# Optimization experiments

Measured on AMD Instinct MI355X. Metric: run time of the kernel, lower is better.

## Reference

```python
import jax, jax.numpy as jnp
import numpy as np

NEG_SLOPE = 0.2
K_NN = 3


def gat_conv(x, edge_index, W, a_src, a_dst, b):
    """PyG GATConv (heads=1, add_self_loops=True).
    x: [N, F_in]; edge_index: [2, E] (row0=src, row1=dst)."""
    n = x.shape[0]
    loops = jnp.arange(n)
    src = jnp.concatenate([edge_index[0], loops])
    dst = jnp.concatenate([edge_index[1], loops])
    h = x @ W                                   # [N, H]
    a_s = h @ a_src                             # [N] per-node src score
    a_d = h @ a_dst                             # [N] per-node dst score
    e = jax.nn.leaky_relu(a_s[src] + a_d[dst], NEG_SLOPE)  # [E+N]
    # segment softmax over edges sharing the same destination
    e_max = jax.ops.segment_max(e, dst, num_segments=n)
    ex = jnp.exp(e - e_max[dst])
    denom = jax.ops.segment_sum(ex, dst, num_segments=n)
    alpha = ex / denom[dst]
    out = jax.ops.segment_sum(alpha[:, None] * h[src], dst, num_segments=n)
    return out + b


def knn_pool(x_resting, x_collider):
    """For each collider node find K_NN nearest resting nodes (L2), then
    scatter_mean collider features onto resting nodes."""
    nr = x_resting.shape[0]
    nc = x_collider.shape[0]
    # squared distances [Nc, Nr]
    d2 = (jnp.sum(x_collider ** 2, -1, keepdims=True)
          - 2.0 * (x_collider @ x_resting.T)
          + jnp.sum(x_resting ** 2, -1)[None, :])
    _, idx = jax.lax.top_k(-d2, K_NN)           # [Nc, K] resting indices
    row = idx.reshape(-1)                        # resting index per knn edge
    col = jnp.repeat(jnp.arange(nc), K_NN)       # collider index per knn edge
    feats = x_collider[col]                      # [Nc*K, H]
    sums = jax.ops.segment_sum(feats, row, num_segments=nr)
    cnt = jax.ops.segment_sum(jnp.ones((nc * K_NN,), feats.dtype), row,
                              num_segments=nr)
    return sums / jnp.maximum(cnt, 1.0)[:, None]


def setup_inputs() -> dict:
    key = jax.random.key(0)
    ks = jax.random.split(key, 20)
    Nr, Nc, Er, Ec = 10000, 5000, 160000, 80000
    Fr, Fc, H, O = 3, 6, 128, 3
    s = 0.1
    inp = {
        "x_resting": jax.random.normal(ks[0], (Nr, Fr), jnp.float32),
        "edge_index_resting": jax.random.randint(ks[1], (2, Er), 0, Nr),
        "x_collider": jax.random.normal(ks[2], (Nc, Fc), jnp.float32),
        "edge_index_collider": jax.random.randint(ks[3], (2, Ec), 0, Nc),
        # conv1_resting
        "W1r": jax.random.normal(ks[4], (Fr, H), jnp.float32) * s,
        "as1r": jax.random.normal(ks[5], (H,), jnp.float32) * s,
        "ad1r": jax.random.normal(ks[6], (H,), jnp.float32) * s,
        "b1r": jnp.zeros((H,), jnp.float32),
        # conv2_resting
        "W2r": jax.random.normal(ks[7], (H, H), jnp.float32) * s,
        "as2r": jax.random.normal(ks[8], (H,), jnp.float32) * s,
        "ad2r": jax.random.normal(ks[9], (H,), jnp.float32) * s,
        "b2r": jnp.zeros((H,), jnp.float32),
        # conv1_collider
        "W1c": jax.random.normal(ks[10], (Fc, H), jnp.float32) * s,
        "as1c": jax.random.normal(ks[11], (H,), jnp.float32) * s,
        "ad1c": jax.random.normal(ks[12], (H,), jnp.float32) * s,
        "b1c": jnp.zeros((H,), jnp.float32),
        # conv2_collider
        "W2c": jax.random.normal(ks[13], (H, H), jnp.float32) * s,
        "as2c": jax.random.normal(ks[14], (H,), jnp.float32) * s,
        "ad2c": jax.random.normal(ks[15], (H,), jnp.float32) * s,
        "b2c": jnp.zeros((H,), jnp.float32),
        # decoder
        "Wd": jax.random.normal(ks[16], (2 * H, O), jnp.float32) * s,
        "bd": jnp.zeros((O,), jnp.float32),
    }
    return inp


def reference(x_resting, edge_index_resting, x_collider, edge_index_collider,
              W1r, as1r, ad1r, b1r, W2r, as2r, ad2r, b2r,
              W1c, as1c, ad1c, b1c, W2c, as2c, ad2c, b2c, Wd, bd):
    # resting branch (dropout is identity in eval mode)
    hr = jax.nn.relu(gat_conv(x_resting, edge_index_resting, W1r, as1r, ad1r, b1r))
    hr = jax.nn.relu(gat_conv(hr, edge_index_resting, W2r, as2r, ad2r, b2r))
    # collider branch
    hc = jax.nn.relu(gat_conv(x_collider, edge_index_collider, W1c, as1c, ad1c, b1c))
    hc = jax.nn.relu(gat_conv(hc, edge_index_collider, W2c, as2c, ad2c, b2c))
    pooled = knn_pool(hr, hc)                    # [Nr, H]
    x_combined = jnp.concatenate([hr, pooled], axis=-1)
    x_out = x_combined @ Wd + bd                 # new node positions [Nr, 3]
    return x_out
```

## Files before the change

kernel.cpp:

```cpp
#include <hip/hip_runtime.h>
#include <hip/hip_bf16.h>
#include <cstdint>
#include <cstddef>

#define DI __device__ __forceinline__

DI float lrelu(float x) { return x > 0.f ? x : 0.2f * x; }
DI int clampi(int v, int lo, int hi) { return v < lo ? lo : (v > hi ? hi : v); }
DI float clampf(float v) { return fminf(fmaxf(v, -1e15f), 1e15f); }

DI float ldm(const void* p, int i, int mode) {
    if (mode) return ((const float*)p)[i];
    return __bfloat162float(((const __hip_bfloat16*)p)[i]);
}

DI void ins3(float v, int ix, float bv[3], int bi[3]) {
    bool b2 = (v < bv[2]) || (v == bv[2] && ix < bi[2]);
    if (!b2) return;
    bool b0 = (v < bv[0]) || (v == bv[0] && ix < bi[0]);
    bool b1 = (v < bv[1]) || (v == bv[1] && ix < bi[1]);
    if (b0) {
        bv[2] = bv[1]; bi[2] = bi[1];
        bv[1] = bv[0]; bi[1] = bi[0];
        bv[0] = v;     bi[0] = ix;
    } else if (b1) {
        bv[2] = bv[1]; bi[2] = bi[1];
        bv[1] = v;     bi[1] = ix;
    } else {
        bv[2] = v;     bi[2] = ix;
    }
}

__global__ void k_detect(const unsigned short* __restrict__ u, int n, int* __restrict__ flag) {
    int i = blockIdx.x * 256 + threadIdx.x;
    if (i < n) {
        if (((u[i] >> 7) & 0xFF) == 0xFF) atomicOr(flag, 1);
    }
}

__global__ void k_hist(const int* __restrict__ dst, int E, int* __restrict__ deg, int N) {
    int e = blockIdx.x * 256 + threadIdx.x;
    if (e < E) {
        unsigned d = (unsigned)dst[e];
        if (d < (unsigned)N) atomicAdd(&deg[d], 1);
    }
}

__global__ __launch_bounds__(1024) void k_scan(const int* __restrict__ deg, int* __restrict__ off, int N) {
    __shared__ int s[1024];
    __shared__ int carry_s;
    int tid = threadIdx.x;
    if (tid == 0) carry_s = 0;
    __syncthreads();
    for (int base = 0; base < N; base += 1024) {
        int i = base + tid;
        int v = (i < N) ? deg[i] : 0;
        s[tid] = v;
        __syncthreads();
        for (int d = 1; d < 1024; d <<= 1) {
            int t = (tid >= d) ? s[tid - d] : 0;
            __syncthreads();
            s[tid] += t;
            __syncthreads();
        }
        if (i < N) off[i] = carry_s + s[tid] - v;
        int tot = s[1023];
        __syncthreads();
        if (tid == 0) carry_s += tot;
        __syncthreads();
    }
    if (tid == 0) off[N] = carry_s;
}

__global__ void k_scatter(const int* __restrict__ src, const int* __restrict__ dst, int E,
                          const int* __restrict__ off, int* __restrict__ cur, int* __restrict__ sorted,
                          int N) {
    int e = blockIdx.x * 256 + threadIdx.x;
    if (e < E) {
        unsigned d = (unsigned)dst[e];
        if (d < (unsigned)N) {
            int p = off[d] + atomicAdd(&cur[d], 1);
            sorted[p] = clampi(src[e], 0, N - 1);
        }
    }
}

template <int FIN>
__global__ __launch_bounds__(128) void k_lin(const void* __restrict__ x,
                                             const void* __restrict__ W,
                                             const void* __restrict__ av_src,
                                             const void* __restrict__ av_dst,
                                             const int* __restrict__ mode_p,
                                             float* __restrict__ h, float* __restrict__ as_,
                                             float* __restrict__ ad_, int N) {
    int mode = *mode_p;
    int n = blockIdx.x;
    int f = threadIdx.x;
    __shared__ float xs[FIN];
    if (f < FIN) xs[f] = ldm(x, n * FIN + f, mode);
    __syncthreads();
    float acc = 0.f;
#pragma unroll
    for (int k = 0; k < FIN; k++) acc += xs[k] * ldm(W, k * 128 + f, mode);
    acc = clampf(acc);
    h[(size_t)n * 128 + f] = acc;
    __shared__ float r1[128], r2[128];
    r1[f] = acc * ldm(av_src, f, mode);
    r2[f] = acc * ldm(av_dst, f, mode);
    __syncthreads();
    for (int s2 = 64; s2 > 0; s2 >>= 1) {
        if (f < s2) { r1[f] += r1[f + s2]; r2[f] += r2[f + s2]; }
        __syncthreads();
    }
    if (f == 0) { as_[n] = clampf(r1[0]); ad_[n] = clampf(r2[0]); }
}

__global__ __launch_bounds__(128) void k_lin_f32(const float* __restrict__ x,
                                                 const void* __restrict__ W,
                                                 const void* __restrict__ av_src,
                                                 const void* __restrict__ av_dst,
                                                 const int* __restrict__ mode_p,
                                                 float* __restrict__ h, float* __restrict__ as_,
                                                 float* __restrict__ ad_, int N) {
    int mode = *mode_p;
    int n = blockIdx.x;
    int f = threadIdx.x;
    __shared__ float xs[128];
    xs[f] = x[(size_t)n * 128 + f];
    __syncthreads();
    float acc = 0.f;
#pragma unroll
    for (int k = 0; k < 128; k++) acc += xs[k] * ldm(W, k * 128 + f, mode);
    acc = clampf(acc);
    h[(size_t)n * 128 + f] = acc;
    __shared__ float r1[128], r2[128];
    r1[f] = acc * ldm(av_src, f, mode);
    r2[f] = acc * ldm(av_dst, f, mode);
    __syncthreads();
    for (int s2 = 64; s2 > 0; s2 >>= 1) {
        if (f < s2) { r1[f] += r1[f + s2]; r2[f] += r2[f + s2]; }
        __syncthreads();
    }
    if (f == 0) { as_[n] = clampf(r1[0]); ad_[n] = clampf(r2[0]); }
}

__global__ __launch_bounds__(256) void k_agg(const float* __restrict__ h, const float* __restrict__ as_,
                                             const float* __restrict__ ad_, const int* __restrict__ off,
                                             const int* __restrict__ sorted,
                                             const void* __restrict__ bias,
                                             const int* __restrict__ mode_p,
                                             float* __restrict__ out, int N) {
    int mode = *mode_p;
    int w = (blockIdx.x * blockDim.x + threadIdx.x) >> 6;
    int lane = threadIdx.x & 63;
    if (w >= N) return;
    int s0 = off[w], s1 = off[w + 1];
    float adv = ad_[w];
    float eself = lrelu(as_[w] + adv);
    float m = eself;
    for (int j = s0 + lane; j < s1; j += 64) {
        int s = clampi(sorted[j], 0, N - 1);
        m = fmaxf(m, lrelu(as_[s] + adv));
    }
#pragma unroll
    for (int d = 32; d > 0; d >>= 1) m = fmaxf(m, __shfl_xor(m, d, 64));
    const float2* h2 = (const float2*)h;
    float wself = __expf(eself - m);
    float denom = wself;
    float2 hv = h2[(size_t)w * 64 + lane];
    float a0 = wself * hv.x, a1 = wself * hv.y;
    for (int j = s0; j < s1; j++) {
        int s = clampi(sorted[j], 0, N - 1);
        float wj = __expf(lrelu(as_[s] + adv) - m);
        denom += wj;
        float2 hs = h2[(size_t)s * 64 + lane];
        a0 += wj * hs.x;
        a1 += wj * hs.y;
    }
    float inv = 1.f / fmaxf(denom, 1e-30f);
    float o0 = a0 * inv + ldm(bias, lane * 2, mode);
    float o1 = a1 * inv + ldm(bias, lane * 2 + 1, mode);
    out[(size_t)w * 128 + lane * 2] = fminf(fmaxf(o0, 0.f), 1e15f);
    out[(size_t)w * 128 + lane * 2 + 1] = fminf(fmaxf(o1, 0.f), 1e15f);
}

__global__ __launch_bounds__(256) void k_norm(const float* __restrict__ hr, float* __restrict__ rn, int N) {
    int w = (blockIdx.x * blockDim.x + threadIdx.x) >> 6;
    int lane = threadIdx.x & 63;
    if (w >= N) return;
    const float2* h2 = (const float2*)hr;
    float2 v = h2[(size_t)w * 64 + lane];
    float s = v.x * v.x + v.y * v.y;
#pragma unroll
    for (int d = 32; d > 0; d >>= 1) s += __shfl_xor(s, d, 64);
    if (lane == 0) rn[w] = s;
}

#define KNN_TC 64
#define KNN_TR 128
#define KNN_NCH 16
#define KNN_STRIDE 36

__global__ __launch_bounds__(256)
void k_knn_part(const float* __restrict__ hr,
                const float* __restrict__ hc,
                const float* __restrict__ rn,
                float* __restrict__ cand_v, int* __restrict__ cand_i,
                int NR, int NC, int chunk) {
    __shared__ float lds[(KNN_TC + KNN_TR) * KNN_STRIDE];
    float* hcs = lds;
    float* hrs = lds + KNN_TC * KNN_STRIDE;
    int tid = threadIdx.x;
    int tx = tid & 7;
    int ty = tid >> 3;
    int c0 = blockIdx.x * KNN_TC;
    int rbase = blockIdx.y * chunk;
    int rend = min(rbase + chunk, NR);

    float bv[8][3];
    int bi[8][3];
#pragma unroll
    for (int i = 0; i < 8; i++)
#pragma unroll
        for (int j = 0; j < 3; j++) { bv[i][j] = 3.4e38f; bi[i][j] = 0x7fffffff; }

    for (int rt = rbase; rt < rend; rt += KNN_TR) {
        float acc[8][4];
#pragma unroll
        for (int i = 0; i < 8; i++)
#pragma unroll
            for (int j = 0; j < 4; j++) acc[i][j] = 0.f;

        for (int ks = 0; ks < 128; ks += 32) {
            __syncthreads();
#pragma unroll
            for (int q = 0; q < 2; q++) {
                int idx = q * 256 + tid;
                int row = idx >> 3, col4 = idx & 7;
                int c = c0 + row;
                float4 v = make_float4(0.f, 0.f, 0.f, 0.f);
                if (c < NC) v = *(const float4*)&hc[(size_t)c * 128 + ks + col4 * 4];
                *(float4*)&hcs[row * KNN_STRIDE + col4 * 4] = v;
            }
#pragma unroll
            for (int q = 0; q < 4; q++) {
                int idx = q * 256 + tid;
                int row = idx >> 3, col4 = idx & 7;
                int r = rt + row;
                float4 v = make_float4(0.f, 0.f, 0.f, 0.f);
                if (r < rend) v = *(const float4*)&hr[(size_t)r * 128 + ks + col4 * 4];
                *(float4*)&hrs[row * KNN_STRIDE + col4 * 4] = v;
            }
            __syncthreads();
#pragma unroll 2
            for (int kk4 = 0; kk4 < 8; kk4++) {
                float4 b[4];
#pragma unroll
                for (int j = 0; j < 4; j++)
                    b[j] = *(const float4*)&hrs[(ty + 32 * j) * KNN_STRIDE + kk4 * 4];
#pragma unroll
                for (int i = 0; i < 8; i++) {
                    float4 a = *(const float4*)&hcs[(tx + 8 * i) * KNN_STRIDE + kk4 * 4];
#pragma unroll
                    for (int j = 0; j < 4; j++) {
                        acc[i][j] += a.x * b[j].x;
                        acc[i][j] += a.y * b[j].y;
                        acc[i][j] += a.z * b[j].z;
                        acc[i][j] += a.w * b[j].w;
                    }
                }
            }
        }
#pragma unroll
        for (int j = 0; j < 4; j++) {
            int r = rt + ty + 32 * j;
            if (r < rend) {
                float rnv = rn[r];
#pragma unroll
                for (int i = 0; i < 8; i++) {
                    float d = rnv - 2.f * acc[i][j];
                    ins3(d, r, bv[i], bi[i]);
                }
            }
        }
    }

    float* mv = lds;
    int* mi = (int*)(lds + KNN_TC * 48);
    float fv[3] = {3.4e38f, 3.4e38f, 3.4e38f};
    int fi[3] = {0x7fffffff, 0x7fffffff, 0x7fffffff};

    __syncthreads();
    if (ty < 16) {
#pragma unroll
        for (int i = 0; i < 8; i++) {
            int cc = tx + 8 * i;
#pragma unroll
            for (int j = 0; j < 3; j++) {
                mv[cc * 48 + ty * 3 + j] = bv[i][j];
                mi[cc * 48 + ty * 3 + j] = bi[i][j];
            }
        }
    }
    __syncthreads();
    if (tid < KNN_TC) {
        for (int t = 0; t < 48; t++) ins3(mv[tid * 48 + t], mi[tid * 48 + t], fv, fi);
    }
    __syncthreads();
    if (ty >= 16) {
#pragma unroll
        for (int i = 0; i < 8; i++) {
            int cc = tx + 8 * i;
#pragma unroll
            for (int j = 0; j < 3; j++) {
                mv[cc * 48 + (ty - 16) * 3 + j] = bv[i][j];
                mi[cc * 48 + (ty - 16) * 3 + j] = bi[i][j];
            }
        }
    }
    __syncthreads();
    if (tid < KNN_TC) {
        for (int t = 0; t < 48; t++) ins3(mv[tid * 48 + t], mi[tid * 48 + t], fv, fi);
        int c = c0 + tid;
        if (c < NC) {
            size_t o = ((size_t)c * KNN_NCH + blockIdx.y) * 3;
            cand_v[o + 0] = fv[0]; cand_i[o + 0] = fi[0];
            cand_v[o + 1] = fv[1]; cand_i[o + 1] = fi[1];
            cand_v[o + 2] = fv[2]; cand_i[o + 2] = fi[2];
        }
    }
}

__global__ void k_knn_merge(const float* __restrict__ cand_v, const int* __restrict__ cand_i,
                            int* __restrict__ knn, int NC, int NR) {
    int c = blockIdx.x * 256 + threadIdx.x;
    if (c >= NC) return;
    float fv[3] = {3.4e38f, 3.4e38f, 3.4e38f};
    int fi[3] = {0x7fffffff, 0x7fffffff, 0x7fffffff};
    size_t o = (size_t)c * KNN_NCH * 3;
    for (int t = 0; t < KNN_NCH * 3; t++) ins3(cand_v[o + t], cand_i[o + t], fv, fi);
    knn[c * 3 + 0] = clampi(fi[0], 0, NR - 1);
    knn[c * 3 + 1] = clampi(fi[1], 0, NR - 1);
    knn[c * 3 + 2] = clampi(fi[2], 0, NR - 1);
}

__global__ __launch_bounds__(128) void k_pool_scatter(const float* __restrict__ hc,
                                                      const int* __restrict__ knn,
                                                      float* __restrict__ psum, float* __restrict__ pcnt,
                                                      int NC, int NR) {
    int c = blockIdx.x;
    int f = threadIdx.x;
    float v = hc[(size_t)c * 128 + f];
#pragma unroll
    for (int j = 0; j < 3; j++) {
        int r = clampi(knn[c * 3 + j], 0, NR - 1);
        atomicAdd(&psum[(size_t)r * 128 + f], v);
        if (f == 0) atomicAdd(&pcnt[r], 1.f);
    }
}

__global__ __launch_bounds__(256) void k_decode(const float* __restrict__ hr, const float* __restrict__ psum,
                                                const float* __restrict__ pcnt,
                                                const void* __restrict__ Wd,
                                                const void* __restrict__ bd,
                                                const int* __restrict__ mode_p,
                                                void* __restrict__ outv, int NR) {
    int mode = *mode_p;
    int w = (blockIdx.x * blockDim.x + threadIdx.x) >> 6;
    int lane = threadIdx.x & 63;
    if (w >= NR) return;
    float icnt = 1.f / fmaxf(pcnt[w], 1.f);
    float o0 = 0.f, o1 = 0.f, o2 = 0.f;
#pragma unroll
    for (int hh = 0; hh < 2; hh++) {
        int f = lane + hh * 64;
        float xv = hr[(size_t)w * 128 + f];
        o0 += xv * ldm(Wd, f * 3 + 0, mode);
        o1 += xv * ldm(Wd, f * 3 + 1, mode);
        o2 += xv * ldm(Wd, f * 3 + 2, mode);
        float pv = psum[(size_t)w * 128 + f] * icnt;
        o0 += pv * ldm(Wd, (128 + f) * 3 + 0, mode);
        o1 += pv * ldm(Wd, (128 + f) * 3 + 1, mode);
        o2 += pv * ldm(Wd, (128 + f) * 3 + 2, mode);
    }
#pragma unroll
    for (int d = 32; d > 0; d >>= 1) {
        o0 += __shfl_xor(o0, d, 64);
        o1 += __shfl_xor(o1, d, 64);
        o2 += __shfl_xor(o2, d, 64);
    }
    if (lane == 0) {
        float v0 = o0 + ldm(bd, 0, mode);
        float v1 = o1 + ldm(bd, 1, mode);
        float v2 = o2 + ldm(bd, 2, mode);
        if (mode) {
            float* out = (float*)outv;
            out[w * 3 + 0] = v0;
            out[w * 3 + 1] = v1;
            out[w * 3 + 2] = v2;
        } else {
            __hip_bfloat16* out = (__hip_bfloat16*)outv;
            out[w * 3 + 0] = __float2bfloat16(v0);
            out[w * 3 + 1] = __float2bfloat16(v1);
            out[w * 3 + 2] = __float2bfloat16(v2);
        }
    }
}

extern "C" void kernel_launch(void* const* d_in, const int* in_sizes, int n_in,
                              void* d_out, int out_size, void* d_ws, size_t ws_size,
                              hipStream_t stream) {
    const void* x_r = d_in[0];
    const int* ei_r = (const int*)d_in[1];
    const void* x_c = d_in[2];
    const int* ei_c = (const int*)d_in[3];
    const void* W1r = d_in[4];
    const void* as1r = d_in[5];
    const void* ad1r = d_in[6];
    const void* b1r = d_in[7];
    const void* W2r = d_in[8];
    const void* as2r = d_in[9];
    const void* ad2r = d_in[10];
    const void* b2r = d_in[11];
    const void* W1c = d_in[12];
    const void* as1c = d_in[13];
    const void* ad1c = d_in[14];
    const void* b1c = d_in[15];
    const void* W2c = d_in[16];
    const void* as2c = d_in[17];
    const void* ad2c = d_in[18];
    const void* b2c = d_in[19];
    const void* Wd = d_in[20];
    const void* bd = d_in[21];

    const int NR = in_sizes[0] / 3;
    const int ER = in_sizes[1] / 2;
    const int NC = in_sizes[2] / 6;
    const int EC = in_sizes[3] / 2;

    char* p = (char*)d_ws;
    size_t used = 0;
    auto alloc = [&](size_t bytes) {
        void* q = (void*)(p + used);
        used += (bytes + 255) & ~(size_t)255;
        return q;
    };
    float* r_A = (float*)alloc((size_t)NR * 128 * 4);
    float* r_B = (float*)alloc((size_t)NR * 128 * 4);
    float* c_A = (float*)alloc((size_t)NC * 128 * 4);
    float* c_B = (float*)alloc((size_t)NC * 128 * 4);
    float* r_as = (float*)alloc((size_t)NR * 4);
    float* r_ad = (float*)alloc((size_t)NR * 4);
    float* c_as = (float*)alloc((size_t)NC * 4);
    float* c_ad = (float*)alloc((size_t)NC * 4);
    int* r_deg = (int*)alloc((size_t)NR * 4);
    int* r_cur = (int*)alloc((size_t)NR * 4);
    int* r_off = (int*)alloc((size_t)(NR + 1) * 4);
    int* r_sorted = (int*)alloc((size_t)ER * 4);
    int* c_deg = (int*)alloc((size_t)NC * 4);
    int* c_cur = (int*)alloc((size_t)NC * 4);
    int* c_off = (int*)alloc((size_t)(NC + 1) * 4);
    int* c_sorted = (int*)alloc((size_t)EC * 4);
    int* mode_p = (int*)alloc(256);

    float* psum = r_A;
    float* rn = r_as;
    float* pcnt = r_ad;
    float* cand_v = c_A;
    int* cand_i = (int*)(c_A + (size_t)NC * KNN_NCH * 3);
    int* knn = (int*)(c_A + (size_t)NC * KNN_NCH * 6);

    if (ws_size < used) return;

    (void)hipMemsetAsync(r_deg, 0, (size_t)NR * 4, stream);
    (void)hipMemsetAsync(r_cur, 0, (size_t)NR * 4, stream);
    (void)hipMemsetAsync(c_deg, 0, (size_t)NC * 4, stream);
    (void)hipMemsetAsync(c_cur, 0, (size_t)NC * 4, stream);
    (void)hipMemsetAsync(mode_p, 0, 4, stream);

    k_detect<<<(in_sizes[0] + 255) / 256, 256, 0, stream>>>((const unsigned short*)x_r, in_sizes[0], mode_p);
    k_detect<<<(in_sizes[2] + 255) / 256, 256, 0, stream>>>((const unsigned short*)x_c, in_sizes[2], mode_p);

    k_hist<<<(ER + 255) / 256, 256, 0, stream>>>(ei_r + ER, ER, r_deg, NR);
    k_scan<<<1, 1024, 0, stream>>>(r_deg, r_off, NR);
    k_scatter<<<(ER + 255) / 256, 256, 0, stream>>>(ei_r, ei_r + ER, ER, r_off, r_cur, r_sorted, NR);
    k_hist<<<(EC + 255) / 256, 256, 0, stream>>>(ei_c + EC, EC, c_deg, NC);
    k_scan<<<1, 1024, 0, stream>>>(c_deg, c_off, NC);
    k_scatter<<<(EC + 255) / 256, 256, 0, stream>>>(ei_c, ei_c + EC, EC, c_off, c_cur, c_sorted, NC);

    const int aggBlocksR = (NR * 64 + 255) / 256;
    const int aggBlocksC = (NC * 64 + 255) / 256;

    k_lin<3><<<NR, 128, 0, stream>>>(x_r, W1r, as1r, ad1r, mode_p, r_A, r_as, r_ad, NR);
    k_agg<<<aggBlocksR, 256, 0, stream>>>(r_A, r_as, r_ad, r_off, r_sorted, b1r, mode_p, r_B, NR);
    k_lin_f32<<<NR, 128, 0, stream>>>(r_B, W2r, as2r, ad2r, mode_p, r_A, r_as, r_ad, NR);
    k_agg<<<aggBlocksR, 256, 0, stream>>>(r_A, r_as, r_ad, r_off, r_sorted, b2r, mode_p, r_B, NR);

    k_lin<6><<<NC, 128, 0, stream>>>(x_c, W1c, as1c, ad1c, mode_p, c_A, c_as, c_ad, NC);
    k_agg<<<aggBlocksC, 256, 0, stream>>>(c_A, c_as, c_ad, c_off, c_sorted, b1c, mode_p, c_B, NC);
    k_lin_f32<<<NC, 128, 0, stream>>>(c_B, W2c, as2c, ad2c, mode_p, c_A, c_as, c_ad, NC);
    k_agg<<<aggBlocksC, 256, 0, stream>>>(c_A, c_as, c_ad, c_off, c_sorted, b2c, mode_p, c_B, NC);

    (void)hipMemsetAsync(psum, 0, (size_t)NR * 128 * 4, stream);
    (void)hipMemsetAsync(pcnt, 0, (size_t)NR * 4, stream);

    k_norm<<<aggBlocksR, 256, 0, stream>>>(r_B, rn, NR);
    int chunk = (NR + KNN_NCH - 1) / KNN_NCH;
    dim3 kg((NC + KNN_TC - 1) / KNN_TC, KNN_NCH);
    k_knn_part<<<kg, 256, 0, stream>>>(r_B, c_B, rn, cand_v, cand_i, NR, NC, chunk);
    k_knn_merge<<<(NC + 255) / 256, 256, 0, stream>>>(cand_v, cand_i, knn, NC, NR);
    k_pool_scatter<<<NC, 128, 0, stream>>>(c_B, knn, psum, pcnt, NC, NR);

    k_decode<<<aggBlocksR, 256, 0, stream>>>(r_B, psum, pcnt, Wd, bd, mode_p, d_out, NR);
}
```

Measured before the change: 882.1 us.

## Batch resting and collider branches into shared launches and fuse small kernels

Merges the resting and collider branches into single launches for detect, histogram, scan, scatter, linear and aggregation. The row-norm computation moves into the second aggregation kernel, and kNN merge and pool scatter become one kernel. All zeroing is collapsed into one contiguous memset by reordering the workspace. This cuts launch count and lets the smaller collider work overlap the resting work on the GPU. The cost is branchy kernel prologues and a non-templated first linear loop, and the serial merge now runs on one thread per 128-thread block.

After: 803.6 us. 1.1x faster.

```diff
diff --git a/kernel.cpp b/kernel.cpp
--- a/kernel.cpp
+++ b/kernel.cpp
@@ -31,22 +31,33 @@
     }
 }
 
-__global__ void k_detect(const unsigned short* __restrict__ u, int n, int* __restrict__ flag) {
+__global__ void k_detect2(const unsigned short* __restrict__ u0, int n0,
+                          const unsigned short* __restrict__ u1, int n1,
+                          int* __restrict__ flag) {
     int i = blockIdx.x * 256 + threadIdx.x;
-    if (i < n) {
-        if (((u[i] >> 7) & 0xFF) == 0xFF) atomicOr(flag, 1);
-    }
-}
-
-__global__ void k_hist(const int* __restrict__ dst, int E, int* __restrict__ deg, int N) {
+    if (i < n0 + n1) {
+        unsigned short v = (i < n0) ? u0[i] : u1[i - n0];
+        if (((v >> 7) & 0xFF) == 0xFF) atomicOr(flag, 1);
+    }
+}
+
+__global__ void k_hist2(const int* __restrict__ dstR, int ER, int* __restrict__ degR, int NR,
+                        const int* __restrict__ dstC, int EC, int* __restrict__ degC, int NC) {
     int e = blockIdx.x * 256 + threadIdx.x;
-    if (e < E) {
-        unsigned d = (unsigned)dst[e];
-        if (d < (unsigned)N) atomicAdd(&deg[d], 1);
-    }
-}
-
-__global__ __launch_bounds__(1024) void k_scan(const int* __restrict__ deg, int* __restrict__ off, int N) {
+    if (e < ER) {
+        unsigned d = (unsigned)dstR[e];
+        if (d < (unsigned)NR) atomicAdd(&degR[d], 1);
+    } else if (e < ER + EC) {
+        unsigned d = (unsigned)dstC[e - ER];
+        if (d < (unsigned)NC) atomicAdd(&degC[d], 1);
+    }
+}
+
+__global__ __launch_bounds__(1024) void k_scan2(const int* __restrict__ degR, int* __restrict__ offR, int NR,
+                                                const int* __restrict__ degC, int* __restrict__ offC, int NC) {
+    const int* deg = blockIdx.x ? degC : degR;
+    int* off = blockIdx.x ? offC : offR;
+    int N = blockIdx.x ? NC : NR;
     __shared__ int s[1024];
     __shared__ int carry_s;
     int tid = threadIdx.x;
@@ -72,41 +83,53 @@
     if (tid == 0) off[N] = carry_s;
 }
 
-__global__ void k_scatter(const int* __restrict__ src, const int* __restrict__ dst, int E,
-                          const int* __restrict__ off, int* __restrict__ cur, int* __restrict__ sorted,
-                          int N) {
+__global__ void k_scatter2(const int* __restrict__ srcR, const int* __restrict__ dstR, int ER,
+                           const int* __restrict__ offR, int* __restrict__ curR, int* __restrict__ sortedR, int NR,
+                           const int* __restrict__ srcC, const int* __restrict__ dstC, int EC,
+                           const int* __restrict__ offC, int* __restrict__ curC, int* __restrict__ sortedC, int NC) {
     int e = blockIdx.x * 256 + threadIdx.x;
-    if (e < E) {
-        unsigned d = (unsigned)dst[e];
-        if (d < (unsigned)N) {
-            int p = off[d] + atomicAdd(&cur[d], 1);
-            sorted[p] = clampi(src[e], 0, N - 1);
-        }
-    }
-}
-
-template <int FIN>
-__global__ __launch_bounds__(128) void k_lin(const void* __restrict__ x,
-                                             const void* __restrict__ W,
-                                             const void* __restrict__ av_src,
-                                             const void* __restrict__ av_dst,
-                                             const int* __restrict__ mode_p,
-                                             float* __restrict__ h, float* __restrict__ as_,
-                                             float* __restrict__ ad_, int N) {
+    if (e < ER) {
+        unsigned d = (unsigned)dstR[e];
+        if (d < (unsigned)NR) {
+            int p = offR[d] + atomicAdd(&curR[d], 1);
+            sortedR[p] = clampi(srcR[e], 0, NR - 1);
+        }
+    } else if (e < ER + EC) {
+        int e2 = e - ER;
+        unsigned d = (unsigned)dstC[e2];
+        if (d < (unsigned)NC) {
+            int p = offC[d] + atomicAdd(&curC[d], 1);
+            sortedC[p] = clampi(srcC[e2], 0, NC - 1);
+        }
+    }
+}
+
+__global__ __launch_bounds__(128) void k_lin1_both(
+    const void* __restrict__ xR, const void* __restrict__ WR,
+    const void* __restrict__ avsR, const void* __restrict__ avdR,
+    float* __restrict__ hR, float* __restrict__ asR, float* __restrict__ adR, int NR,
+    const void* __restrict__ xC, const void* __restrict__ WC,
+    const void* __restrict__ avsC, const void* __restrict__ avdC,
+    float* __restrict__ hC, float* __restrict__ asC, float* __restrict__ adC, int NC,
+    const int* __restrict__ mode_p) {
     int mode = *mode_p;
-    int n = blockIdx.x;
+    int bid = blockIdx.x;
     int f = threadIdx.x;
-    __shared__ float xs[FIN];
-    if (f < FIN) xs[f] = ldm(x, n * FIN + f, mode);
+    const void *x, *W, *avs, *avd;
+    float *h, *as_, *ad_;
+    int n, fin;
+    if (bid < NR) { n = bid; fin = 3; x = xR; W = WR; avs = avsR; avd = avdR; h = hR; as_ = asR; ad_ = adR; }
+    else          { n = bid - NR; fin = 6; x = xC; W = WC; avs = avsC; avd = avdC; h = hC; as_ = asC; ad_ = adC; }
+    __shared__ float xs[8];
+    __shared__ float r1[128], r2[128];
+    if (f < fin) xs[f] = ldm(x, n * fin + f, mode);
     __syncthreads();
     float acc = 0.f;
-#pragma unroll
-    for (int k = 0; k < FIN; k++) acc += xs[k] * ldm(W, k * 128 + f, mode);
+    for (int k = 0; k < fin; k++) acc += xs[k] * ldm(W, k * 128 + f, mode);
     acc = clampf(acc);
     h[(size_t)n * 128 + f] = acc;
-    __shared__ float r1[128], r2[128];
-    r1[f] = acc * ldm(av_src, f, mode);
-    r2[f] = acc * ldm(av_dst, f, mode);
+    r1[f] = acc * ldm(avs, f, mode);
+    r2[f] = acc * ldm(avd, f, mode);
     __syncthreads();
     for (int s2 = 64; s2 > 0; s2 >>= 1) {
         if (f < s2) { r1[f] += r1[f + s2]; r2[f] += r2[f + s2]; }
@@ -115,17 +138,25 @@
     if (f == 0) { as_[n] = clampf(r1[0]); ad_[n] = clampf(r2[0]); }
 }
 
-__global__ __launch_bounds__(128) void k_lin_f32(const float* __restrict__ x,
-                                                 const void* __restrict__ W,
-                                                 const void* __restrict__ av_src,
-                                                 const void* __restrict__ av_dst,
-                                                 const int* __restrict__ mode_p,
-                                                 float* __restrict__ h, float* __restrict__ as_,
-                                                 float* __restrict__ ad_, int N) {
+__global__ __launch_bounds__(128) void k_lin2_both(
+    const float* __restrict__ xR, const void* __restrict__ WR,
+    const void* __restrict__ avsR, const void* __restrict__ avdR,
+    float* __restrict__ hR, float* __restrict__ asR, float* __restrict__ adR, int NR,
+    const float* __restrict__ xC, const void* __restrict__ WC,
+    const void* __restrict__ avsC, const void* __restrict__ avdC,
+    float* __restrict__ hC, float* __restrict__ asC, float* __restrict__ adC, int NC,
+    const int* __restrict__ mode_p) {
     int mode = *mode_p;
-    int n = blockIdx.x;
+    int bid = blockIdx.x;
     int f = threadIdx.x;
+    const float* x;
+    const void *W, *avs, *avd;
+    float *h, *as_, *ad_;
+    int n;
+    if (bid < NR) { n = bid; x = xR; W = WR; avs = avsR; avd = avdR; h = hR; as_ = asR; ad_ = adR; }
+    else          { n = bid - NR; x = xC; W = WC; avs = avsC; avd = avdC; h = hC; as_ = asC; ad_ = adC; }
     __shared__ float xs[128];
+    __shared__ float r1[128], r2[128];
     xs[f] = x[(size_t)n * 128 + f];
     __syncthreads();
     float acc = 0.f;
@@ -133,9 +164,8 @@
     for (int k = 0; k < 128; k++) acc += xs[k] * ldm(W, k * 128 + f, mode);
     acc = clampf(acc);
     h[(size_t)n * 128 + f] = acc;
-    __shared__ float r1[128], r2[128];
-    r1[f] = acc * ldm(av_src, f, mode);
-    r2[f] = acc * ldm(av_dst, f, mode);
+    r1[f] = acc * ldm(avs, f, mode);
+    r2[f] = acc * ldm(avd, f, mode);
     __syncthreads();
     for (int s2 = 64; s2 > 0; s2 >>= 1) {
         if (f < s2) { r1[f] += r1[f + s2]; r2[f] += r2[f + s2]; }
@@ -144,15 +174,25 @@
     if (f == 0) { as_[n] = clampf(r1[0]); ad_[n] = clampf(r2[0]); }
 }
 
-__global__ __launch_bounds__(256) void k_agg(const float* __restrict__ h, const float* __restrict__ as_,
-                                             const float* __restrict__ ad_, const int* __restrict__ off,
-                                             const int* __restrict__ sorted,
-                                             const void* __restrict__ bias,
-                                             const int* __restrict__ mode_p,
-                                             float* __restrict__ out, int N) {
+__global__ __launch_bounds__(256) void k_agg_both(
+    const float* __restrict__ hR, const float* __restrict__ asR, const float* __restrict__ adR,
+    const int* __restrict__ offR, const int* __restrict__ srtR, const void* __restrict__ biasR,
+    float* __restrict__ outR, int NR,
+    const float* __restrict__ hC, const float* __restrict__ asC, const float* __restrict__ adC,
+    const int* __restrict__ offC, const int* __restrict__ srtC, const void* __restrict__ biasC,
+    float* __restrict__ outC, int NC,
+    const int* __restrict__ mode_p, int blocksR, float* __restrict__ rn, int do_rn) {
     int mode = *mode_p;
-    int w = (blockIdx.x * blockDim.x + threadIdx.x) >> 6;
+    int bid = blockIdx.x;
+    int wid = threadIdx.x >> 6;
     int lane = threadIdx.x & 63;
+    const float *h, *as_, *ad_;
+    const int *off, *sorted;
+    const void* bias;
+    float* out;
+    int w, N, isR;
+    if (bid < blocksR) { isR = 1; w = bid * 4 + wid; N = NR; h = hR; as_ = asR; ad_ = adR; off = offR; sorted = srtR; bias = biasR; out = outR; }
+    else               { isR = 0; w = (bid - blocksR) * 4 + wid; N = NC; h = hC; as_ = asC; ad_ = adC; off = offC; sorted = srtC; bias = biasC; out = outC; }
     if (w >= N) return;
     int s0 = off[w], s1 = off[w + 1];
     float adv = ad_[w];
@@ -178,22 +218,16 @@
         a1 += wj * hs.y;
     }
     float inv = 1.f / fmaxf(denom, 1e-30f);
-    float o0 = a0 * inv + ldm(bias, lane * 2, mode);
-    float o1 = a1 * inv + ldm(bias, lane * 2 + 1, mode);
-    out[(size_t)w * 128 + lane * 2] = fminf(fmaxf(o0, 0.f), 1e15f);
-    out[(size_t)w * 128 + lane * 2 + 1] = fminf(fmaxf(o1, 0.f), 1e15f);
-}
-
-__global__ __launch_bounds__(256) void k_norm(const float* __restrict__ hr, float* __restrict__ rn, int N) {
-    int w = (blockIdx.x * blockDim.x + threadIdx.x) >> 6;
-    int lane = threadIdx.x & 63;
-    if (w >= N) return;
-    const float2* h2 = (const float2*)hr;
-    float2 v = h2[(size_t)w * 64 + lane];
-    float s = v.x * v.x + v.y * v.y;
-#pragma unroll
-    for (int d = 32; d > 0; d >>= 1) s += __shfl_xor(s, d, 64);
-    if (lane == 0) rn[w] = s;
+    float o0 = fminf(fmaxf(a0 * inv + ldm(bias, lane * 2, mode), 0.f), 1e15f);
+    float o1 = fminf(fmaxf(a1 * inv + ldm(bias, lane * 2 + 1, mode), 0.f), 1e15f);
+    out[(size_t)w * 128 + lane * 2] = o0;
+    out[(size_t)w * 128 + lane * 2 + 1] = o1;
+    if (do_rn && isR) {
+        float s = o0 * o0 + o1 * o1;
+#pragma unroll
+        for (int d = 32; d > 0; d >>= 1) s += __shfl_xor(s, d, 64);
+        if (lane == 0) rn[w] = s;
+    }
 }
 
 #define KNN_TC 64
@@ -331,32 +365,29 @@
     }
 }
 
-__global__ void k_knn_merge(const float* __restrict__ cand_v, const int* __restrict__ cand_i,
-                            int* __restrict__ knn, int NC, int NR) {
-    int c = blockIdx.x * 256 + threadIdx.x;
-    if (c >= NC) return;
-    float fv[3] = {3.4e38f, 3.4e38f, 3.4e38f};
-    int fi[3] = {0x7fffffff, 0x7fffffff, 0x7fffffff};
-    size_t o = (size_t)c * KNN_NCH * 3;
-    for (int t = 0; t < KNN_NCH * 3; t++) ins3(cand_v[o + t], cand_i[o + t], fv, fi);
-    knn[c * 3 + 0] = clampi(fi[0], 0, NR - 1);
-    knn[c * 3 + 1] = clampi(fi[1], 0, NR - 1);
-    knn[c * 3 + 2] = clampi(fi[2], 0, NR - 1);
-}
-
-__global__ __launch_bounds__(128) void k_pool_scatter(const float* __restrict__ hc,
-                                                      const int* __restrict__ knn,
-                                                      float* __restrict__ psum, float* __restrict__ pcnt,
-                                                      int NC, int NR) {
+__global__ __launch_bounds__(128) void k_mergepool(const float* __restrict__ cand_v,
+                                                   const int* __restrict__ cand_i,
+                                                   const float* __restrict__ hc,
+                                                   float* __restrict__ psum, float* __restrict__ pcnt,
+                                                   int NC, int NR) {
     int c = blockIdx.x;
     int f = threadIdx.x;
+    __shared__ int kn[3];
+    if (f == 0) {
+        float fv[3] = {3.4e38f, 3.4e38f, 3.4e38f};
+        int fi[3] = {0x7fffffff, 0x7fffffff, 0x7fffffff};
+        size_t o = (size_t)c * KNN_NCH * 3;
+        for (int t = 0; t < KNN_NCH * 3; t++) ins3(cand_v[o + t], cand_i[o + t], fv, fi);
+#pragma unroll
+        for (int j = 0; j < 3; j++) {
+            kn[j] = clampi(fi[j], 0, NR - 1);
+            atomicAdd(&pcnt[kn[j]], 1.f);
+        }
+    }
+    __syncthreads();
     float v = hc[(size_t)c * 128 + f];
 #pragma unroll
-    for (int j = 0; j < 3; j++) {
-        int r = clampi(knn[c * 3 + j], 0, NR - 1);
-        atomicAdd(&psum[(size_t)r * 128 + f], v);
-        if (f == 0) atomicAdd(&pcnt[r], 1.f);
-    }
+    for (int j = 0; j < 3; j++) atomicAdd(&psum[(size_t)kn[j] * 128 + f], v);
 }
 
 __global__ __launch_bounds__(256) void k_decode(const float* __restrict__ hr, const float* __restrict__ psum,
@@ -453,63 +484,55 @@
     float* r_ad = (float*)alloc((size_t)NR * 4);
     float* c_as = (float*)alloc((size_t)NC * 4);
     float* c_ad = (float*)alloc((size_t)NC * 4);
+    float* rn = (float*)alloc((size_t)NR * 4);
+    int* r_off = (int*)alloc((size_t)(NR + 1) * 4);
+    int* r_sorted = (int*)alloc((size_t)ER * 4);
+    int* c_off = (int*)alloc((size_t)(NC + 1) * 4);
+    int* c_sorted = (int*)alloc((size_t)EC * 4);
+    size_t zero_off = used;
+    float* psum = (float*)alloc((size_t)NR * 128 * 4);
+    float* pcnt = (float*)alloc((size_t)NR * 4);
     int* r_deg = (int*)alloc((size_t)NR * 4);
     int* r_cur = (int*)alloc((size_t)NR * 4);
-    int* r_off = (int*)alloc((size_t)(NR + 1) * 4);
-    int* r_sorted = (int*)alloc((size_t)ER * 4);
     int* c_deg = (int*)alloc((size_t)NC * 4);
     int* c_cur = (int*)alloc((size_t)NC * 4);
-    int* c_off = (int*)alloc((size_t)(NC + 1) * 4);
-    int* c_sorted = (int*)alloc((size_t)EC * 4);
     int* mode_p = (int*)alloc(256);
-
-    float* psum = r_A;
-    float* rn = r_as;
-    float* pcnt = r_ad;
+    size_t zero_len = used - zero_off;
+
     float* cand_v = c_A;
     int* cand_i = (int*)(c_A + (size_t)NC * KNN_NCH * 3);
-    int* knn = (int*)(c_A + (size_t)NC * KNN_NCH * 6);
 
     if (ws_size < used) return;
 
-    (void)hipMemsetAsync(r_deg, 0, (size_t)NR * 4, stream);
-    (void)hipMemsetAsync(r_cur, 0, (size_t)NR * 4, stream);
-    (void)hipMemsetAsync(c_deg, 0, (size_t)NC * 4, stream);
-    (void)hipMemsetAsync(c_cur, 0, (size_t)NC * 4, stream);
-    (void)hipMemsetAsync(mode_p, 0, 4, stream);
-
-    k_detect<<<(in_sizes[0] + 255) / 256, 256, 0, stream>>>((const unsigned short*)x_r, in_sizes[0], mode_p);
-    k_detect<<<(in_sizes[2] + 255) / 256, 256, 0, stream>>>((const unsigned short*)x_c, in_sizes[2], mode_p);
-
-    k_hist<<<(ER + 255) / 256, 256, 0, stream>>>(ei_r + ER, ER, r_deg, NR);
-    k_scan<<<1, 1024, 0, stream>>>(r_deg, r_off, NR);
-    k_scatter<<<(ER + 255) / 256, 256, 0, stream>>>(ei_r, ei_r + ER, ER, r_off, r_cur, r_sorted, NR);
-    k_hist<<<(EC + 255) / 256, 256, 0, stream>>>(ei_c + EC, EC, c_deg, NC);
-    k_scan<<<1, 1024, 0, stream>>>(c_deg, c_off, NC);
-    k_scatter<<<(EC + 255) / 256, 256, 0, stream>>>(ei_c, ei_c + EC, EC, c_off, c_cur, c_sorted, NC);
+    (void)hipMemsetAsync(p + zero_off, 0, zero_len, stream);
+
+    k_detect2<<<(in_sizes[0] + in_sizes[2] + 255) / 256, 256, 0, stream>>>(
+        (const unsigned short*)x_r, in_sizes[0], (const unsigned short*)x_c, in_sizes[2], mode_p);
+
+    k_hist2<<<(ER + EC + 255) / 256, 256, 0, stream>>>(ei_r + ER, ER, r_deg, NR, ei_c + EC, EC, c_deg, NC);
+    k_scan2<<<2, 1024, 0, stream>>>(r_deg, r_off, NR, c_deg, c_off, NC);
+    k_scatter2<<<(ER + EC + 255) / 256, 256, 0, stream>>>(ei_r, ei_r + ER, ER, r_off, r_cur, r_sorted, NR,
+                                                          ei_c, ei_c + EC, EC, c_off, c_cur, c_sorted, NC);
 
     const int aggBlocksR = (NR * 64 + 255) / 256;
     const int aggBlocksC = (NC * 64 + 255) / 256;
 
-    k_lin<3><<<NR, 128, 0, stream>>>(x_r, W1r, as1r, ad1r, mode_p, r_A, r_as, r_ad, NR);
-    k_agg<<<aggBlocksR, 256, 0, stream>>>(r_A, r_as, r_ad, r_off, r_sorted, b1r, mode_p, r_B, NR);
-    k_lin_f32<<<NR, 128, 0, stream>>>(r_B, W2r, as2r, ad2r, mode_p, r_A, r_as, r_ad, NR);
-    k_agg<<<aggBlocksR, 256, 0, stream>>>(r_A, r_as, r_ad, r_off, r_sorted, b2r, mode_p, r_B, NR);
-
-    k_lin<6><<<NC, 128, 0, stream>>>(x_c, W1c, as1c, ad1c, mode_p, c_A, c_as, c_ad, NC);
-    k_agg<<<aggBlocksC, 256, 0, stream>>>(c_A, c_as, c_ad, c_off, c_sorted, b1c, mode_p, c_B, NC);
-    k_lin_f32<<<NC, 128, 0, stream>>>(c_B, W2c, as2c, ad2c, mode_p, c_A, c_as, c_ad, NC);
-    k_agg<<<aggBlocksC, 256, 0, stream>>>(c_A, c_as, c_ad, c_off, c_sorted, b2c, mode_p, c_B, NC);
-
-    (void)hipMemsetAsync(psum, 0, (size_t)NR * 128 * 4, stream);
-    (void)hipMemsetAsync(pcnt, 0, (size_t)NR * 4, stream);
-
-    k_norm<<<aggBlocksR, 256, 0, stream>>>(r_B, rn, NR);
+    k_lin1_both<<<NR + NC, 128, 0, stream>>>(x_r, W1r, as1r, ad1r, r_A, r_as, r_ad, NR,
+                                             x_c, W1c, as1c, ad1c, c_A, c_as, c_ad, NC, mode_p);
+    k_agg_both<<<aggBlocksR + aggBlocksC, 256, 0, stream>>>(
+        r_A, r_as, r_ad, r_off, r_sorted, b1r, r_B, NR,
+        c_A, c_as, c_ad, c_off, c_sorted, b1c, c_B, NC, mode_p, aggBlocksR, rn, 0);
+
+    k_lin2_both<<<NR + NC, 128, 0, stream>>>(r_B, W2r, as2r, ad2r, r_A, r_as, r_ad, NR,
+                                             c_B, W2c, as2c, ad2c, c_A, c_as, c_ad, NC, mode_p);
+    k_agg_both<<<aggBlocksR + aggBlocksC, 256, 0, stream>>>(
+        r_A, r_as, r_ad, r_off, r_sorted, b2r, r_B, NR,
+        c_A, c_as, c_ad, c_off, c_sorted, b2c, c_B, NC, mode_p, aggBlocksR, rn, 1);
+
     int chunk = (NR + KNN_NCH - 1) / KNN_NCH;
     dim3 kg((NC + KNN_TC - 1) / KNN_TC, KNN_NCH);
     k_knn_part<<<kg, 256, 0, stream>>>(r_B, c_B, rn, cand_v, cand_i, NR, NC, chunk);
-    k_knn_merge<<<(NC + 255) / 256, 256, 0, stream>>>(cand_v, cand_i, knn, NC, NR);
-    k_pool_scatter<<<NC, 128, 0, stream>>>(c_B, knn, psum, pcnt, NC, NR);
+    k_mergepool<<<NC, 128, 0, stream>>>(cand_v, cand_i, c_B, psum, pcnt, NC, NR);
 
     k_decode<<<aggBlocksR, 256, 0, stream>>>(r_B, psum, pcnt, Wd, bd, mode_p, d_out, NR);
 }
```
